# Optimization experiments

Measured on AMD Instinct MI355X. Metric: run time of the kernel, lower is better.

## Reference

```python
import jax, jax.numpy as jnp
import numpy as np

NUM_USER = 100000
NUM_ITEM = 50000
N = NUM_USER + NUM_ITEM
E = 1200000
D = 64          # emb_size
F_ITEM = 384    # raw item multimodal feature dim
K = 3           # number of global embedding rows (summed over dim 0)
N_LAYERS = 4
EPS = 1e-8      # F.cosine_similarity default eps


def setup_inputs() -> dict:
    key = jax.random.key(0)
    ks = jax.random.split(key, 9)
    return {
        "adj_row": jax.random.randint(ks[0], (E,), 0, N),
        "adj_col": jax.random.randint(ks[1], (E,), 0, N),
        # scaled like a degree-normalized adjacency (avg degree ~8)
        "adj_val": jax.random.uniform(ks[2], (E,), jnp.float32) / 8.0,
        "user_fea": jax.random.normal(ks[3], (NUM_USER, D), jnp.float32) * 0.1,
        "item_fea": jax.random.normal(ks[4], (NUM_ITEM, F_ITEM), jnp.float32) * 0.1,
        "g_emb_u": jax.random.normal(ks[5], (K, D), jnp.float32) * 0.1,
        "g_emb_i": jax.random.normal(ks[6], (K, D), jnp.float32) * 0.1,
        "mlp_w": jax.random.normal(ks[7], (D, F_ITEM), jnp.float32) * (1.0 / np.sqrt(F_ITEM)),
        "mlp_b": jnp.zeros((D,), jnp.float32),
    }


def _cosine_sim(a, b):
    # matches F.cosine_similarity(a, b, dim=-1) with eps clamp on norms
    na = jnp.maximum(jnp.linalg.norm(a, axis=-1), EPS)
    nb = jnp.maximum(jnp.linalg.norm(b, axis=-1), EPS)
    return jnp.sum(a * b, axis=-1) / (na * nb)


def reference(adj_row, adj_col, adj_val, user_fea, item_fea, g_emb_u, g_emb_i, mlp_w, mlp_b):
    # global embeddings summed over modality dim
    user_emb = user_fea + jnp.sum(g_emb_u, axis=0)                       # [U, D]
    item_emb = jnp.tanh(item_fea @ mlp_w.T + mlp_b) + jnp.sum(g_emb_i, axis=0)  # [I, D]
    ego = jnp.concatenate([user_emb, item_emb], axis=0)                  # [N, D]

    x = ego
    acc = ego  # sum over layers, includes layer-0 (ego) term
    for _ in range(N_LAYERS):
        # sparse adj @ x as gather -> scale -> segment-sum scatter
        x = jax.ops.segment_sum(adj_val[:, None] * x[adj_col], adj_row, num_segments=N)
        w = _cosine_sim(x, ego)     # [N]
        x = w[:, None] * x          # einsum('a,ab->ab')
        acc = acc + x

    return acc[:NUM_USER], acc[NUM_USER:]
```

## Files before the change

kernel.cpp:

```cpp
#include <hip/hip_runtime.h>
#include <hip/hip_bf16.h>

#define U_NUM 100000
#define I_NUM 50000
#define N_NUM 150000
#define E_NUM 1200000
#define D 64
#define F_IT 384
#define CAP 32
#define EPSV 1e-8f
#define FXS 524288.0f
#define FXI (1.0f / 524288.0f)

#define NBIN 586
#define RPB 256
#define FBLK 1172
#define CELL_CAP 8
#define OV_CAP 64

typedef unsigned short ushort_t;
typedef unsigned int uint_t;
typedef short bf16x8 __attribute__((ext_vector_type(8)));
typedef float f32x4 __attribute__((ext_vector_type(4)));

__device__ __forceinline__ ushort_t f2bf(float f) {
    uint_t x = __float_as_uint(f);
    uint_t r = x + 0x7fffu + ((x >> 16) & 1u);
    return (ushort_t)(r >> 16);
}
__device__ __forceinline__ float bfu2f(uint_t u_lo16) {
    return __uint_as_float(u_lo16 << 16);
}
__device__ __forceinline__ void dec8(uint4 u, float* f) {
    f[0] = bfu2f(u.x & 0xffffu); f[1] = bfu2f(u.x >> 16);
    f[2] = bfu2f(u.y & 0xffffu); f[3] = bfu2f(u.y >> 16);
    f[4] = bfu2f(u.z & 0xffffu); f[5] = bfu2f(u.z >> 16);
    f[6] = bfu2f(u.w & 0xffffu); f[7] = bfu2f(u.w >> 16);
}

__global__ void k_prep(const float* __restrict__ w, const float* __restrict__ gu,
                       const float* __restrict__ gi,
                       short* __restrict__ wbf, float* __restrict__ gsu,
                       float* __restrict__ gsi, int* __restrict__ ovcnt) {
    int b = blockIdx.x, t = threadIdx.x;
    if (b < 96) {
        int i = b * 256 + t;
        wbf[i] = (short)f2bf(w[i]);
    } else {
        if (t < 64) gsu[t] = gu[t] + gu[64 + t] + gu[128 + t];
        else if (t < 128) { int d = t - 64; gsi[d] = gi[d] + gi[64 + d] + gi[128 + d]; }
        for (int i = t; i < NBIN; i += 256) ovcnt[i] = 0;
    }
}

__global__ __launch_bounds__(256) void k_fill(
        const int* __restrict__ row, const int* __restrict__ col,
        const float* __restrict__ val,
        int2* __restrict__ cellbuf, int* __restrict__ cellcnt,
        int* __restrict__ ovcnt, int2* __restrict__ ovbuf) {
    __shared__ int bincnt[NBIN];
    int fid = blockIdx.x, tid = threadIdx.x;
    for (int i = tid; i < NBIN; i += 256) bincnt[i] = 0;
    __syncthreads();
    int t = fid * 256 + tid;
    if (t < E_NUM / 4) {
        int r[4], c[4];
        float v[4];
#pragma unroll
        for (int k = 0; k < 4; k++) {
            int e = k * (E_NUM / 4) + t;
            r[k] = row[e]; c[k] = col[e]; v[k] = val[e];
        }
#pragma unroll
        for (int k = 0; k < 4; k++) {
            int bn = r[k] >> 8;
            int key = c[k] | ((r[k] & 255) << 18);
            int ls = atomicAdd(&bincnt[bn], 1);
            if (ls < CELL_CAP) {
                cellbuf[((size_t)fid * NBIN + bn) * CELL_CAP + ls] =
                    make_int2(key, __float_as_int(v[k]));
            } else {
                int o = atomicAdd(&ovcnt[bn], 1);
                if (o < OV_CAP) ovbuf[bn * OV_CAP + o] = make_int2(key, __float_as_int(v[k]));
            }
        }
    }
    __syncthreads();
    for (int i = tid; i < NBIN; i += 256)
        cellcnt[(size_t)fid * NBIN + i] = min(bincnt[i], CELL_CAP);
}

#define ITEM_B 782
__global__ __launch_bounds__(256) void k_item(
        const float* __restrict__ ifea, const float* __restrict__ bvec,
        const short* __restrict__ wbf, const float* __restrict__ gsi,
        float* __restrict__ ego, ushort_t* __restrict__ egob) {
    int iid = blockIdx.x;
    int tid = threadIdx.x;
    int wave = tid >> 6, lane = tid & 63;
    int q = lane >> 4, m = lane & 15;
    int ibase = iid * 64 + wave * 16;
    int irow = min(ibase + m, I_NUM - 1);
    const float* arow = ifea + (size_t)irow * F_IT + q * 8;

    f32x4 av[4];
#pragma unroll
    for (int n = 0; n < 4; n++) av[n] = (f32x4){0.f, 0.f, 0.f, 0.f};
    float4 nfa0 = ((const float4*)(arow))[0];
    float4 nfa1 = ((const float4*)(arow))[1];
#pragma unroll
    for (int c = 0; c < 12; c++) {
        float4 fa0 = nfa0, fa1 = nfa1;
        if (c < 11) {
            nfa0 = ((const float4*)(arow + (c + 1) * 32))[0];
            nfa1 = ((const float4*)(arow + (c + 1) * 32))[1];
        }
        bf16x8 af;
        af[0] = (short)f2bf(fa0.x); af[1] = (short)f2bf(fa0.y);
        af[2] = (short)f2bf(fa0.z); af[3] = (short)f2bf(fa0.w);
        af[4] = (short)f2bf(fa1.x); af[5] = (short)f2bf(fa1.y);
        af[6] = (short)f2bf(fa1.z); af[7] = (short)f2bf(fa1.w);
#pragma unroll
        for (int n = 0; n < 4; n++) {
            bf16x8 bf = *(const bf16x8*)(wbf + (size_t)(n * 16 + m) * F_IT + c * 32 + q * 8);
            av[n] = __builtin_amdgcn_mfma_f32_16x16x32_bf16(af, bf, av[n], 0, 0, 0);
        }
    }
#pragma unroll
    for (int n = 0; n < 4; n++) {
        int dim = n * 16 + m;
        float bb = bvec[dim];
        float gg = gsi[dim];
#pragma unroll
        for (int rr = 0; rr < 4; rr++) {
            int item = ibase + q * 4 + rr;
            if (item < I_NUM) {
                float v = tanhf(av[n][rr] + bb) + gg;
                size_t o = (size_t)(U_NUM + item) * D + dim;
                ego[o] = v;
                egob[o] = f2bf(v);
            }
        }
    }
}

#define USER_B 1563
__global__ __launch_bounds__(256) void k_user(
        const float* __restrict__ ufea, const float* __restrict__ gsu,
        float* __restrict__ ego, ushort_t* __restrict__ egob) {
    int t = blockIdx.x * 256 + threadIdx.x;
    size_t base = (size_t)t * 16;
    if (base >= (size_t)U_NUM * D) return;
    int d0 = (int)(base & 63);
    float f[16];
#pragma unroll
    for (int k = 0; k < 4; k++) {
        float4 v = ((const float4*)(ufea + base))[k];
        f[4 * k] = v.x; f[4 * k + 1] = v.y; f[4 * k + 2] = v.z; f[4 * k + 3] = v.w;
    }
#pragma unroll
    for (int j = 0; j < 16; j++) f[j] += gsu[d0 + j];
#pragma unroll
    for (int k = 0; k < 4; k++) {
        ((float4*)(ego + base))[k] = make_float4(f[4 * k], f[4 * k + 1], f[4 * k + 2], f[4 * k + 3]);
    }
    uint4 u0, u1;
    u0.x = (uint_t)f2bf(f[0]) | ((uint_t)f2bf(f[1]) << 16);
    u0.y = (uint_t)f2bf(f[2]) | ((uint_t)f2bf(f[3]) << 16);
    u0.z = (uint_t)f2bf(f[4]) | ((uint_t)f2bf(f[5]) << 16);
    u0.w = (uint_t)f2bf(f[6]) | ((uint_t)f2bf(f[7]) << 16);
    u1.x = (uint_t)f2bf(f[8]) | ((uint_t)f2bf(f[9]) << 16);
    u1.y = (uint_t)f2bf(f[10]) | ((uint_t)f2bf(f[11]) << 16);
    u1.z = (uint_t)f2bf(f[12]) | ((uint_t)f2bf(f[13]) << 16);
    u1.w = (uint_t)f2bf(f[14]) | ((uint_t)f2bf(f[15]) << 16);
    ((uint4*)(egob + base))[0] = u0;
    ((uint4*)(egob + base))[1] = u1;
}

__global__ __launch_bounds__(256) void k_bucket(const int2* __restrict__ cellbuf,
                                                const int* __restrict__ cellcnt,
                                                const int* __restrict__ ovcnt,
                                                const int2* __restrict__ ovbuf,
                                                int* __restrict__ cnt,
                                                int* __restrict__ colsA,
                                                float* __restrict__ valsA) {
    __shared__ int lc[RPB];
    int bn = blockIdx.x, tid = threadIdx.x;
    lc[tid] = 0;
    __syncthreads();
    int rbase = bn << 8;
#pragma unroll
    for (int h = 0; h < 5; h++) {
        int f = h * 256 + tid;
        if (f < FBLK) {
            int c = cellcnt[(size_t)f * NBIN + bn];
            const int2* cp = cellbuf + ((size_t)f * NBIN + bn) * CELL_CAP;
            for (int i = 0; i < c; i++) {
                int2 e = cp[i];
                int rl = e.x >> 18;
                int s = atomicAdd(&lc[rl], 1);
                if (s < CAP) {
                    size_t o = (size_t)(rbase + rl) * CAP + s;
                    colsA[o] = e.x & 0x3ffff;
                    valsA[o] = __int_as_float(e.y);
                }
            }
        }
    }
    int oc = min(ovcnt[bn], OV_CAP);
    for (int i = tid; i < oc; i += 256) {
        int2 e = ovbuf[bn * OV_CAP + i];
        int rl = e.x >> 18;
        int s = atomicAdd(&lc[rl], 1);
        if (s < CAP) {
            size_t o = (size_t)(rbase + rl) * CAP + s;
            colsA[o] = e.x & 0x3ffff;
            valsA[o] = __int_as_float(e.y);
        }
    }
    __syncthreads();
    int r = rbase + tid;
    if (r < N_NUM) {
        int d = min(lc[tid], CAP);
        int dp = (d + 7) & ~7;
        for (int s = d; s < dp; s++) {
            size_t o = (size_t)r * CAP + s;
            colsA[o] = 0;
            valsA[o] = 0.f;
        }
        cnt[r] = dp;
    }
}

#define ACC8(A, VS, X) \
    A[0] += __float2int_rn(VS * bfu2f(X.x & 0xffffu)); A[1] += __float2int_rn(VS * bfu2f(X.x >> 16)); \
    A[2] += __float2int_rn(VS * bfu2f(X.y & 0xffffu)); A[3] += __float2int_rn(VS * bfu2f(X.y >> 16)); \
    A[4] += __float2int_rn(VS * bfu2f(X.z & 0xffffu)); A[5] += __float2int_rn(VS * bfu2f(X.z >> 16)); \
    A[6] += __float2int_rn(VS * bfu2f(X.w & 0xffffu)); A[7] += __float2int_rn(VS * bfu2f(X.w >> 16));

__device__ __forceinline__ float row_weight(const float* a, const float* e) {
    float dot = 0.f, nx = 0.f, ne = 0.f;
#pragma unroll
    for (int j = 0; j < 8; j++) {
        dot += a[j] * e[j]; nx += a[j] * a[j]; ne += e[j] * e[j];
    }
#pragma unroll
    for (int m = 1; m < 8; m <<= 1) {
        dot += __shfl_xor(dot, m);
        nx  += __shfl_xor(nx, m);
        ne  += __shfl_xor(ne, m);
    }
    return dot / (fmaxf(sqrtf(nx), EPSV) * fmaxf(sqrtf(ne), EPSV));
}

__device__ __forceinline__ void gather_row(const ushort_t* __restrict__ xb,
                                           const int* __restrict__ colsA,
                                           const float* __restrict__ valsA,
                                           int r, int nch, int l, int* __restrict__ a) {
#pragma unroll
    for (int j = 0; j < 8; j++) a[j] = 0;
    const int4*   cp = (const int4*)(colsA + (size_t)r * CAP);
    const float4* vp = (const float4*)(valsA + (size_t)r * CAP);
#pragma unroll
    for (int k = 0; k < 4; k++) {
        if (k < nch) {
            int4   c03 = cp[2 * k], c47 = cp[2 * k + 1];
            float4 v03 = vp[2 * k], v47 = vp[2 * k + 1];
            uint4 xu[8];
            xu[0] = ((const uint4*)xb)[(size_t)c03.x * 8 + l];
            xu[1] = ((const uint4*)xb)[(size_t)c03.y * 8 + l];
            xu[2] = ((const uint4*)xb)[(size_t)c03.z * 8 + l];
            xu[3] = ((const uint4*)xb)[(size_t)c03.w * 8 + l];
            xu[4] = ((const uint4*)xb)[(size_t)c47.x * 8 + l];
            xu[5] = ((const uint4*)xb)[(size_t)c47.y * 8 + l];
            xu[6] = ((const uint4*)xb)[(size_t)c47.z * 8 + l];
            xu[7] = ((const uint4*)xb)[(size_t)c47.w * 8 + l];
            float vs0 = v03.x * FXS, vs1 = v03.y * FXS, vs2 = v03.z * FXS, vs3 = v03.w * FXS;
            float vs4 = v47.x * FXS, vs5 = v47.y * FXS, vs6 = v47.z * FXS, vs7 = v47.w * FXS;
            ACC8(a, vs0, xu[0]); ACC8(a, vs1, xu[1]);
            ACC8(a, vs2, xu[2]); ACC8(a, vs3, xu[3]);
            ACC8(a, vs4, xu[4]); ACC8(a, vs5, xu[5]);
            ACC8(a, vs6, xu[6]); ACC8(a, vs7, xu[7]);
        }
    }
}

__device__ __forceinline__ void spmm_body(const ushort_t* __restrict__ xb,
                                          const ushort_t* __restrict__ egob,
                                          const int* __restrict__ cnt,
                                          const int* __restrict__ colsA,
                                          const float* __restrict__ valsA,
                                          ushort_t* __restrict__ xob) {
    int t = blockIdx.x * 256 + threadIdx.x;
    int l = t & 7, r = t >> 3;
    if (r >= N_NUM) return;
    int nch = cnt[r] >> 3;
    int a[8];
    gather_row(xb, colsA, valsA, r, nch, l, a);
    float af[8];
#pragma unroll
    for (int j = 0; j < 8; j++) af[j] = (float)a[j] * FXI;
    float e[8]; dec8(((const uint4*)egob)[(size_t)r * 8 + l], e);
    float wgt = row_weight(af, e);
    uint4 ov;
    ov.x = (uint_t)f2bf(wgt * af[0]) | ((uint_t)f2bf(wgt * af[1]) << 16);
    ov.y = (uint_t)f2bf(wgt * af[2]) | ((uint_t)f2bf(wgt * af[3]) << 16);
    ov.z = (uint_t)f2bf(wgt * af[4]) | ((uint_t)f2bf(wgt * af[5]) << 16);
    ov.w = (uint_t)f2bf(wgt * af[6]) | ((uint_t)f2bf(wgt * af[7]) << 16);
    ((uint4*)xob)[(size_t)r * 8 + l] = ov;
}

__global__ __launch_bounds__(256, 5) void k_spmmA(const ushort_t* __restrict__ xb,
        const ushort_t* __restrict__ egob, const int* __restrict__ cnt,
        const int* __restrict__ colsA, const float* __restrict__ valsA,
        ushort_t* __restrict__ xob) { spmm_body(xb, egob, cnt, colsA, valsA, xob); }

__global__ __launch_bounds__(256, 5) void k_spmmB(const ushort_t* __restrict__ xb,
        const ushort_t* __restrict__ egob, const int* __restrict__ cnt,
        const int* __restrict__ colsA, const float* __restrict__ valsA,
        ushort_t* __restrict__ xob) { spmm_body(xb, egob, cnt, colsA, valsA, xob); }

__global__ __launch_bounds__(256, 5) void k_spmmC(const ushort_t* __restrict__ xb,
        const ushort_t* __restrict__ egob, const int* __restrict__ cnt,
        const int* __restrict__ colsA, const float* __restrict__ valsA,
        ushort_t* __restrict__ xob) { spmm_body(xb, egob, cnt, colsA, valsA, xob); }

__global__ __launch_bounds__(256, 5) void k_spmm4(const ushort_t* __restrict__ x3,
                                                  const ushort_t* __restrict__ x1,
                                                  const ushort_t* __restrict__ x2,
                                                  const float* __restrict__ ego,
                                                  const int* __restrict__ cnt,
                                                  const int* __restrict__ colsA,
                                                  const float* __restrict__ valsA,
                                                  float* __restrict__ out) {
    int t = blockIdx.x * 256 + threadIdx.x;
    int l = t & 7, r = t >> 3;
    if (r >= N_NUM) return;
    int nch = cnt[r] >> 3;
    int a[8];
    gather_row(x3, colsA, valsA, r, nch, l, a);
    float af[8];
#pragma unroll
    for (int j = 0; j < 8; j++) af[j] = (float)a[j] * FXI;
    size_t rb = (size_t)r * D + l * 8;
    float e[8];
    float4 e0 = ((const float4*)(ego + rb))[0];
    float4 e1 = ((const float4*)(ego + rb))[1];
    e[0] = e0.x; e[1] = e0.y; e[2] = e0.z; e[3] = e0.w;
    e[4] = e1.x; e[5] = e1.y; e[6] = e1.z; e[7] = e1.w;
    float wgt = row_weight(af, e);
    float x1d[8], x2d[8], x3d[8];
    dec8(((const uint4*)x1)[(size_t)r * 8 + l], x1d);
    dec8(((const uint4*)x2)[(size_t)r * 8 + l], x2d);
    dec8(((const uint4*)x3)[(size_t)r * 8 + l], x3d);
    float s[8];
#pragma unroll
    for (int j = 0; j < 8; j++) s[j] = e[j] + x1d[j] + x2d[j] + x3d[j] + wgt * af[j];
    ((float4*)(out + rb))[0] = make_float4(s[0], s[1], s[2], s[3]);
    ((float4*)(out + rb))[1] = make_float4(s[4], s[5], s[6], s[7]);
}

extern "C" void kernel_launch(void* const* d_in, const int* in_sizes, int n_in,
                              void* d_out, int out_size, void* d_ws, size_t ws_size,
                              hipStream_t stream) {
    const int*   adj_row  = (const int*)d_in[0];
    const int*   adj_col  = (const int*)d_in[1];
    const float* adj_val  = (const float*)d_in[2];
    const float* user_fea = (const float*)d_in[3];
    const float* item_fea = (const float*)d_in[4];
    const float* gu       = (const float*)d_in[5];
    const float* gi       = (const float*)d_in[6];
    const float* mlp_w    = (const float*)d_in[7];
    const float* mlp_b    = (const float*)d_in[8];

    float* out = (float*)d_out;

    char* ws = (char*)d_ws;
    size_t off = 0;
    float*    ego  = (float*)(ws + off);    off += (size_t)N_NUM * D * 4;
    ushort_t* egob = (ushort_t*)(ws + off); off += (size_t)N_NUM * D * 2;
    size_t x1off = off;
    ushort_t* x1   = (ushort_t*)(ws + off); off += (size_t)N_NUM * D * 2;
    ushort_t* x2   = (ushort_t*)(ws + off); off += (size_t)N_NUM * D * 2;
    ushort_t* x3   = (ushort_t*)(ws + off); off += (size_t)N_NUM * D * 2;
    int*      cnt  = (int*)(ws + off);      off += (size_t)N_NUM * 4;
    short*    wbf  = (short*)(ws + off);    off += (size_t)D * F_IT * 2;
    float*    gsu  = (float*)(ws + off);    off += 64 * 4;
    float*    gsi  = (float*)(ws + off);    off += 64 * 4;
    off = (off + 255) & ~(size_t)255;
    int*      colsA = (int*)(ws + off);     off += (size_t)N_NUM * CAP * 4;
    float*    valsA = (float*)(ws + off);   off += (size_t)N_NUM * CAP * 4;
    int*      cellcnt = (int*)(ws + off);   off += (size_t)FBLK * NBIN * 4;
    int*      ovcnt   = (int*)(ws + off);   off += (size_t)NBIN * 4;
    int2*     ovbuf   = (int2*)(ws + off);  off += (size_t)NBIN * OV_CAP * 8;
    int2*     cellbuf = (int2*)(ws + x1off);

    k_prep<<<97, 256, 0, stream>>>(mlp_w, gu, gi, wbf, gsu, gsi, ovcnt);
    k_fill<<<FBLK, 256, 0, stream>>>(adj_row, adj_col, adj_val,
                                     cellbuf, cellcnt, ovcnt, ovbuf);
    k_item<<<ITEM_B, 256, 0, stream>>>(item_fea, mlp_b, wbf, gsi, ego, egob);
    k_user<<<USER_B, 256, 0, stream>>>(user_fea, gsu, ego, egob);
    k_bucket<<<NBIN, 256, 0, stream>>>(cellbuf, cellcnt, ovcnt, ovbuf,
                                       cnt, colsA, valsA);
    int g = ((size_t)N_NUM * 8 + 255) / 256;
    k_spmmA<<<g, 256, 0, stream>>>(egob, egob, cnt, colsA, valsA, x1);
    k_spmmB<<<g, 256, 0, stream>>>(x1,   egob, cnt, colsA, valsA, x2);
    k_spmmC<<<g, 256, 0, stream>>>(x2,   egob, cnt, colsA, valsA, x3);
    k_spmm4<<<g, 256, 0, stream>>>(x3, x1, x2, ego, cnt, colsA, valsA, out);
}
```

Baseline: 442.7 us.

## Interleave column/value pairs in bucket storage and halve fill block count

Replaces the separate colsA/valsA arrays with a single interleaved int2 bucket array, so each SpMM row loads its column indices and values from one contiguous region. It also halves the number of fill blocks by having each thread process 8 edges instead of 4, which shrinks the cellcnt/cellbuf scan in k_bucket. To absorb the larger per-block cell overflow, the overflow buffer capacity goes from 64 to 256. More edges per fill block means more overflow traffic through global atomics, and the doubled bucket record size does not change total bytes moved.

```diff
diff --git a/kernel.cpp b/kernel.cpp
--- a/kernel.cpp
+++ b/kernel.cpp
@@ -14,9 +14,9 @@
 
 #define NBIN 586
 #define RPB 256
-#define FBLK 1172
+#define FBLK 586
 #define CELL_CAP 8
-#define OV_CAP 64
+#define OV_CAP 256
 
 typedef unsigned short ushort_t;
 typedef unsigned int uint_t;
@@ -63,16 +63,16 @@
     for (int i = tid; i < NBIN; i += 256) bincnt[i] = 0;
     __syncthreads();
     int t = fid * 256 + tid;
-    if (t < E_NUM / 4) {
-        int r[4], c[4];
-        float v[4];
-#pragma unroll
-        for (int k = 0; k < 4; k++) {
-            int e = k * (E_NUM / 4) + t;
+    if (t < E_NUM / 8) {
+        int r[8], c[8];
+        float v[8];
+#pragma unroll
+        for (int k = 0; k < 8; k++) {
+            int e = k * (E_NUM / 8) + t;
             r[k] = row[e]; c[k] = col[e]; v[k] = val[e];
         }
 #pragma unroll
-        for (int k = 0; k < 4; k++) {
+        for (int k = 0; k < 8; k++) {
             int bn = r[k] >> 8;
             int key = c[k] | ((r[k] & 255) << 18);
             int ls = atomicAdd(&bincnt[bn], 1);
@@ -182,15 +182,14 @@
                                                 const int* __restrict__ ovcnt,
                                                 const int2* __restrict__ ovbuf,
                                                 int* __restrict__ cnt,
-                                                int* __restrict__ colsA,
-                                                float* __restrict__ valsA) {
+                                                int2* __restrict__ bkt) {
     __shared__ int lc[RPB];
     int bn = blockIdx.x, tid = threadIdx.x;
     lc[tid] = 0;
     __syncthreads();
     int rbase = bn << 8;
 #pragma unroll
-    for (int h = 0; h < 5; h++) {
+    for (int h = 0; h < 3; h++) {
         int f = h * 256 + tid;
         if (f < FBLK) {
             int c = cellcnt[(size_t)f * NBIN + bn];
@@ -199,11 +198,7 @@
                 int2 e = cp[i];
                 int rl = e.x >> 18;
                 int s = atomicAdd(&lc[rl], 1);
-                if (s < CAP) {
-                    size_t o = (size_t)(rbase + rl) * CAP + s;
-                    colsA[o] = e.x & 0x3ffff;
-                    valsA[o] = __int_as_float(e.y);
-                }
+                if (s < CAP) bkt[(size_t)(rbase + rl) * CAP + s] = make_int2(e.x & 0x3ffff, e.y);
             }
         }
     }
@@ -212,22 +207,15 @@
         int2 e = ovbuf[bn * OV_CAP + i];
         int rl = e.x >> 18;
         int s = atomicAdd(&lc[rl], 1);
-        if (s < CAP) {
-            size_t o = (size_t)(rbase + rl) * CAP + s;
-            colsA[o] = e.x & 0x3ffff;
-            valsA[o] = __int_as_float(e.y);
-        }
+        if (s < CAP) bkt[(size_t)(rbase + rl) * CAP + s] = make_int2(e.x & 0x3ffff, e.y);
     }
     __syncthreads();
     int r = rbase + tid;
     if (r < N_NUM) {
         int d = min(lc[tid], CAP);
         int dp = (d + 7) & ~7;
-        for (int s = d; s < dp; s++) {
-            size_t o = (size_t)r * CAP + s;
-            colsA[o] = 0;
-            valsA[o] = 0.f;
-        }
+        for (int s = d; s < dp; s++)
+            bkt[(size_t)r * CAP + s] = make_int2(0, 0);
         cnt[r] = dp;
     }
 }
@@ -254,29 +242,31 @@
 }
 
 __device__ __forceinline__ void gather_row(const ushort_t* __restrict__ xb,
-                                           const int* __restrict__ colsA,
-                                           const float* __restrict__ valsA,
-                                           int r, int nch, int l, int* __restrict__ a) {
+                                           const int2* __restrict__ bp,
+                                           int nch, int l, int* __restrict__ a) {
 #pragma unroll
     for (int j = 0; j < 8; j++) a[j] = 0;
-    const int4*   cp = (const int4*)(colsA + (size_t)r * CAP);
-    const float4* vp = (const float4*)(valsA + (size_t)r * CAP);
+    const int4* cp = (const int4*)bp;
 #pragma unroll
     for (int k = 0; k < 4; k++) {
         if (k < nch) {
-            int4   c03 = cp[2 * k], c47 = cp[2 * k + 1];
-            float4 v03 = vp[2 * k], v47 = vp[2 * k + 1];
+            int4 p01 = cp[4 * k + 0];
+            int4 p23 = cp[4 * k + 1];
+            int4 p45 = cp[4 * k + 2];
+            int4 p67 = cp[4 * k + 3];
             uint4 xu[8];
-            xu[0] = ((const uint4*)xb)[(size_t)c03.x * 8 + l];
-            xu[1] = ((const uint4*)xb)[(size_t)c03.y * 8 + l];
-            xu[2] = ((const uint4*)xb)[(size_t)c03.z * 8 + l];
-            xu[3] = ((const uint4*)xb)[(size_t)c03.w * 8 + l];
-            xu[4] = ((const uint4*)xb)[(size_t)c47.x * 8 + l];
-            xu[5] = ((const uint4*)xb)[(size_t)c47.y * 8 + l];
-            xu[6] = ((const uint4*)xb)[(size_t)c47.z * 8 + l];
-            xu[7] = ((const uint4*)xb)[(size_t)c47.w * 8 + l];
-            float vs0 = v03.x * FXS, vs1 = v03.y * FXS, vs2 = v03.z * FXS, vs3 = v03.w * FXS;
-            float vs4 = v47.x * FXS, vs5 = v47.y * FXS, vs6 = v47.z * FXS, vs7 = v47.w * FXS;
+            xu[0] = ((const uint4*)xb)[(size_t)p01.x * 8 + l];
+            xu[1] = ((const uint4*)xb)[(size_t)p01.z * 8 + l];
+            xu[2] = ((const uint4*)xb)[(size_t)p23.x * 8 + l];
+            xu[3] = ((const uint4*)xb)[(size_t)p23.z * 8 + l];
+            xu[4] = ((const uint4*)xb)[(size_t)p45.x * 8 + l];
+            xu[5] = ((const uint4*)xb)[(size_t)p45.z * 8 + l];
+            xu[6] = ((const uint4*)xb)[(size_t)p67.x * 8 + l];
+            xu[7] = ((const uint4*)xb)[(size_t)p67.z * 8 + l];
+            float vs0 = __int_as_float(p01.y) * FXS, vs1 = __int_as_float(p01.w) * FXS;
+            float vs2 = __int_as_float(p23.y) * FXS, vs3 = __int_as_float(p23.w) * FXS;
+            float vs4 = __int_as_float(p45.y) * FXS, vs5 = __int_as_float(p45.w) * FXS;
+            float vs6 = __int_as_float(p67.y) * FXS, vs7 = __int_as_float(p67.w) * FXS;
             ACC8(a, vs0, xu[0]); ACC8(a, vs1, xu[1]);
             ACC8(a, vs2, xu[2]); ACC8(a, vs3, xu[3]);
             ACC8(a, vs4, xu[4]); ACC8(a, vs5, xu[5]);
@@ -288,15 +278,14 @@
 __device__ __forceinline__ void spmm_body(const ushort_t* __restrict__ xb,
                                           const ushort_t* __restrict__ egob,
                                           const int* __restrict__ cnt,
-                                          const int* __restrict__ colsA,
-                                          const float* __restrict__ valsA,
+                                          const int2* __restrict__ bkt,
                                           ushort_t* __restrict__ xob) {
     int t = blockIdx.x * 256 + threadIdx.x;
     int l = t & 7, r = t >> 3;
     if (r >= N_NUM) return;
     int nch = cnt[r] >> 3;
     int a[8];
-    gather_row(xb, colsA, valsA, r, nch, l, a);
+    gather_row(xb, bkt + (size_t)r * CAP, nch, l, a);
     float af[8];
 #pragma unroll
     for (int j = 0; j < 8; j++) af[j] = (float)a[j] * FXI;
@@ -312,33 +301,32 @@
 
 __global__ __launch_bounds__(256, 5) void k_spmmA(const ushort_t* __restrict__ xb,
         const ushort_t* __restrict__ egob, const int* __restrict__ cnt,
-        const int* __restrict__ colsA, const float* __restrict__ valsA,
-        ushort_t* __restrict__ xob) { spmm_body(xb, egob, cnt, colsA, valsA, xob); }
+        const int2* __restrict__ bkt, ushort_t* __restrict__ xob)
+{ spmm_body(xb, egob, cnt, bkt, xob); }
 
 __global__ __launch_bounds__(256, 5) void k_spmmB(const ushort_t* __restrict__ xb,
         const ushort_t* __restrict__ egob, const int* __restrict__ cnt,
-        const int* __restrict__ colsA, const float* __restrict__ valsA,
-        ushort_t* __restrict__ xob) { spmm_body(xb, egob, cnt, colsA, valsA, xob); }
+        const int2* __restrict__ bkt, ushort_t* __restrict__ xob)
+{ spmm_body(xb, egob, cnt, bkt, xob); }
 
 __global__ __launch_bounds__(256, 5) void k_spmmC(const ushort_t* __restrict__ xb,
         const ushort_t* __restrict__ egob, const int* __restrict__ cnt,
-        const int* __restrict__ colsA, const float* __restrict__ valsA,
-        ushort_t* __restrict__ xob) { spmm_body(xb, egob, cnt, colsA, valsA, xob); }
+        const int2* __restrict__ bkt, ushort_t* __restrict__ xob)
+{ spmm_body(xb, egob, cnt, bkt, xob); }
 
 __global__ __launch_bounds__(256, 5) void k_spmm4(const ushort_t* __restrict__ x3,
                                                   const ushort_t* __restrict__ x1,
                                                   const ushort_t* __restrict__ x2,
                                                   const float* __restrict__ ego,
                                                   const int* __restrict__ cnt,
-                                                  const int* __restrict__ colsA,
-                                                  const float* __restrict__ valsA,
+                                                  const int2* __restrict__ bkt,
                                                   float* __restrict__ out) {
     int t = blockIdx.x * 256 + threadIdx.x;
     int l = t & 7, r = t >> 3;
     if (r >= N_NUM) return;
     int nch = cnt[r] >> 3;
     int a[8];
-    gather_row(x3, colsA, valsA, r, nch, l, a);
+    gather_row(x3, bkt + (size_t)r * CAP, nch, l, a);
     float af[8];
 #pragma unroll
     for (int j = 0; j < 8; j++) af[j] = (float)a[j] * FXI;
@@ -388,8 +376,7 @@
     float*    gsu  = (float*)(ws + off);    off += 64 * 4;
     float*    gsi  = (float*)(ws + off);    off += 64 * 4;
     off = (off + 255) & ~(size_t)255;
-    int*      colsA = (int*)(ws + off);     off += (size_t)N_NUM * CAP * 4;
-    float*    valsA = (float*)(ws + off);   off += (size_t)N_NUM * CAP * 4;
+    int2*     bkt  = (int2*)(ws + off);     off += (size_t)N_NUM * CAP * 8;
     int*      cellcnt = (int*)(ws + off);   off += (size_t)FBLK * NBIN * 4;
     int*      ovcnt   = (int*)(ws + off);   off += (size_t)NBIN * 4;
     int2*     ovbuf   = (int2*)(ws + off);  off += (size_t)NBIN * OV_CAP * 8;
@@ -400,11 +387,10 @@
                                      cellbuf, cellcnt, ovcnt, ovbuf);
     k_item<<<ITEM_B, 256, 0, stream>>>(item_fea, mlp_b, wbf, gsi, ego, egob);
     k_user<<<USER_B, 256, 0, stream>>>(user_fea, gsu, ego, egob);
-    k_bucket<<<NBIN, 256, 0, stream>>>(cellbuf, cellcnt, ovcnt, ovbuf,
-                                       cnt, colsA, valsA);
+    k_bucket<<<NBIN, 256, 0, stream>>>(cellbuf, cellcnt, ovcnt, ovbuf, cnt, bkt);
     int g = ((size_t)N_NUM * 8 + 255) / 256;
-    k_spmmA<<<g, 256, 0, stream>>>(egob, egob, cnt, colsA, valsA, x1);
-    k_spmmB<<<g, 256, 0, stream>>>(x1,   egob, cnt, colsA, valsA, x2);
-    k_spmmC<<<g, 256, 0, stream>>>(x2,   egob, cnt, colsA, valsA, x3);
-    k_spmm4<<<g, 256, 0, stream>>>(x3, x1, x2, ego, cnt, colsA, valsA, out);
-}
+    k_spmmA<<<g, 256, 0, stream>>>(egob, egob, cnt, bkt, x1);
+    k_spmmB<<<g, 256, 0, stream>>>(x1,   egob, cnt, bkt, x2);
+    k_spmmC<<<g, 256, 0, stream>>>(x2,   egob, cnt, bkt, x3);
+    k_spmm4<<<g, 256, 0, stream>>>(x3, x1, x2, ego, cnt, bkt, out);
+}
```

Result: faster. 398.4 us (-10.0%).
